# Performance work log

Measured on AMD Instinct MI355X. Metric: run time of the kernel, lower is better.

The kernel has to match this reference:

```python
import jax, jax.numpy as jnp
import numpy as np
from jax import lax

# config constants (match init_kwargs)
SEQ_LEN = 512
PRED_LEN = 96
ENC_IN = 64
D_MODEL = 128
E_LAYERS = 2
GRAPH_SCALE = 16
GRAPH_RANK = 8
TCN_KERNEL = 3
TCN_DILATION = 2
BATCH = 16


def setup_inputs() -> dict:
    key = jax.random.key(0)
    ks = jax.random.split(key, 12)
    s = 0.02
    inp = {
        "x_enc": jax.random.normal(ks[0], (BATCH, SEQ_LEN, ENC_IN), jnp.float32),
        "x_mark_enc": jnp.zeros((BATCH, SEQ_LEN, 4), jnp.float32),
        "x_dec": jnp.zeros((BATCH, PRED_LEN, ENC_IN), jnp.float32),
        "x_mark_dec": jnp.zeros((BATCH, PRED_LEN, 4), jnp.float32),
        # value embedding (scalar -> d_model)
        "w_emb": jax.random.normal(ks[1], (1, D_MODEL), jnp.float32) * s,
        "b_emb": jnp.zeros((D_MODEL,), jnp.float32),
        # stacked dilated causal conv layers [L, K, Cin, Cout]
        "conv_w": jax.random.normal(ks[2], (E_LAYERS, TCN_KERNEL, D_MODEL, D_MODEL), jnp.float32) * s,
        "conv_b": jnp.zeros((E_LAYERS, D_MODEL), jnp.float32),
        # low-rank graph generator projections
        "gg_w1": jax.random.normal(ks[3], (D_MODEL, GRAPH_RANK), jnp.float32) * s,
        "gg_b1": jnp.zeros((GRAPH_RANK,), jnp.float32),
        "gg_w2": jax.random.normal(ks[4], (D_MODEL, GRAPH_RANK), jnp.float32) * s,
        "gg_b2": jnp.zeros((GRAPH_RANK,), jnp.float32),
        # head: Linear(d_model * num_tokens, pred_len)
        "head_w": jax.random.normal(ks[5], (D_MODEL * SEQ_LEN, PRED_LEN), jnp.float32) * s,
        "head_b": jnp.zeros((PRED_LEN,), jnp.float32),
    }
    return inp


def _tcn(x_enc, w_emb, b_emb, conv_w, conv_b):
    # x_enc: [B, L, N] -> channel-independent per-variable encoding -> [B, N, L, D]
    B, L, N = x_enc.shape
    h = x_enc.transpose(0, 2, 1).reshape(B * N, L, 1) @ w_emb + b_emb  # [B*N, L, D]
    for i in range(conv_w.shape[0]):
        dil = TCN_DILATION ** i
        pad = (TCN_KERNEL - 1) * dil
        hp = jnp.pad(h, ((0, 0), (pad, 0), (0, 0)))  # causal left pad
        y = lax.conv_general_dilated(
            hp, conv_w[i], window_strides=(1,), padding="VALID",
            rhs_dilation=(dil,), dimension_numbers=("NWC", "WIO", "NWC"),
        ) + conv_b[i]
        h = jax.nn.gelu(y) + h  # residual
    return h.reshape(B, N, L, -1)


def _forward(x_enc, w_emb, b_emb, conv_w, conv_b, gg_w1, gg_b1, gg_w2, gg_b2, head_w, head_b):
    h_time = _tcn(x_enc, w_emb, b_emb, conv_w, conv_b)  # [B, N, L, D]
    B, N, L, D = h_time.shape
    S = L // GRAPH_SCALE  # number of segments (L divisible by scale)
    h_seg = h_time.reshape(B, N, S, GRAPH_SCALE, D)
    z = h_seg.mean(axis=3)  # [B, N, S, D] segment summaries
    # low-rank graph generation for all segments at once
    e1 = z @ gg_w1 + gg_b1  # [B, N, S, r]
    e2 = z @ gg_w2 + gg_b2
    scores = jnp.einsum("bnsr,bmsr->bsnm", e1, e2) / jnp.asarray(np.sqrt(GRAPH_RANK), z.dtype)
    adj = jax.nn.softmax(scores, axis=-1)  # [B, S, N, N] row-stochastic
    # adjacency temporal-smoothness regularizer: sum_s mean|adj_s - adj_{s-1}|
    reg = jnp.sum(jnp.mean(jnp.abs(adj[:, 1:] - adj[:, :-1]), axis=(0, 2, 3)))
    # graph-weighted feature mixing per segment
    h_mix = jnp.einsum("bsnm,bmscd->bnscd", adj, h_seg).reshape(B, N, L, D)
    # head over flattened (token, dim)
    out = h_mix.reshape(B, N, L * D) @ head_w + head_b  # [B, N, pred_len]
    return out.transpose(0, 2, 1), reg  # [B, pred_len, N]


def reference(x_enc, x_mark_enc, x_dec, x_mark_dec, w_emb, b_emb, conv_w, conv_b,
              gg_w1, gg_b1, gg_w2, gg_b2, head_w, head_b):
    # x_mark_enc / x_dec / x_mark_dec are unused by forecast path (faithful to source)
    return _forward(x_enc, w_emb, b_emb, conv_w, conv_b, gg_w1, gg_b1, gg_w2, gg_b2, head_w, head_b)
```

## Files before the change

kernel.cpp:

```cpp
#include <hip/hip_runtime.h>
#include <hip/hip_bf16.h>


#define BATCH 16
#define SEQ 512
#define NVAR 64
#define DM 128
#define SEG 32
#define SCL 16
#define RNK 8
#define PRED 96
#define BN (BATCH * NVAR)
#define ROWLEN (SEQ * DM)

typedef unsigned short ushort_t;
typedef __attribute__((ext_vector_type(8))) short short8;
typedef __attribute__((ext_vector_type(4))) float f32x4;

__device__ inline float bf2f(ushort_t u) {
    union { unsigned int i; float f; } x;
    x.i = ((unsigned int)u) << 16;
    return x.f;
}
__device__ inline ushort_t f2bf(float f) {
    union { float f; unsigned int i; } u;
    u.f = f;
    unsigned int x = u.i;
    return (ushort_t)((x + 0x7fffu + ((x >> 16) & 1u)) >> 16);
}
__device__ inline unsigned int pkbf(float a, float b) {
    __hip_bfloat162 h = __float22bfloat162_rn(make_float2(a, b));
    union { __hip_bfloat162 h2; unsigned int u; } c;
    c.h2 = h;
    return c.u;
}
__device__ inline float blo(unsigned int u) {
    union { unsigned int i; float f; } x;
    x.i = u << 16;
    return x.f;
}
__device__ inline float bhi(unsigned int u) {
    union { unsigned int i; float f; } x;
    x.i = u & 0xFFFF0000u;
    return x.f;
}
__device__ inline float gelu_fast(float x) {
    float t = 0.7978845608028654f * x * (1.0f + 0.044715f * x * x);
    float e = __expf(-2.0f * t);
    return x * __builtin_amdgcn_rcpf(1.0f + e);
}

__global__ __launch_bounds__(128) void wt_prep(
    const float* __restrict__ conv_w, ushort_t* __restrict__ WTf,
    float* __restrict__ regacc) {
    if (blockIdx.x == 0 && blockIdx.y == 0 && threadIdx.x == 0) regacc[0] = 0.f;
    int lt = blockIdx.x;
    int ci = blockIdx.y;
    int co = threadIdx.x;
    int kt = ci >> 5, quad = (ci >> 3) & 3, j = ci & 7;
    int ng = co >> 4, col = co & 15;
    int lane = quad * 16 + col;
    WTf[((((size_t)lt * 4 + kt) * 8 + ng) * 64 + lane) * 8 + j] =
        f2bf(conv_w[(size_t)lt * 16384 + (size_t)ci * 128 + co]);
}

__global__ __launch_bounds__(256, 4) void tcn_mfma(
    const float* __restrict__ x, const float* __restrict__ w_emb,
    const float* __restrict__ b_emb, const ushort_t* __restrict__ WTf,
    const float* __restrict__ conv_b,
    const float* __restrict__ gw1, const float* __restrict__ gb1,
    const float* __restrict__ gw2, const float* __restrict__ gb2,
    ushort_t* __restrict__ h2, float* __restrict__ e1, float* __restrict__ e2) {
    __shared__ __align__(16) ushort_t h0s[82 * 136];
    __shared__ __align__(16) ushort_t h1b[68 * 136];
    float* zb = reinterpret_cast<float*>(h1b);

    int bn = blockIdx.x;
    int b = bn >> 6, n = bn & 63;
    int chunk = blockIdx.y;
    int l0 = chunk * 64;

    {
        const float* xb = x + (size_t)b * SEQ * NVAR + n;
#pragma unroll
        for (int i = 0; i < 21; ++i) {
            int q = threadIdx.x + 256 * i;
            if (q < 82 * 64) {
                int row = q >> 6, dp = (q & 63) * 2;
                int l = l0 + row - 18;
                unsigned int pk = 0;
                if (l >= 0) {
                    float xv = xb[(size_t)l * NVAR];
                    float2 wv2 = *reinterpret_cast<const float2*>(&w_emb[dp]);
                    float2 bv2 = *reinterpret_cast<const float2*>(&b_emb[dp]);
                    pk = pkbf(xv * wv2.x + bv2.x, xv * wv2.y + bv2.y);
                }
                *reinterpret_cast<unsigned int*>(&h0s[row * 136 + dp]) = pk;
            }
        }
    }
    __syncthreads();

    int lane = threadIdx.x & 63;
    int wv = threadIdx.x >> 6;
    int quad = lane >> 4;
    int col = lane & 15;
    int cobase = wv * 32;

    f32x4 acc1[5][2];
#pragma unroll
    for (int mt = 0; mt < 5; ++mt)
#pragma unroll
        for (int nt = 0; nt < 2; ++nt)
            acc1[mt][nt] = (f32x4){0.f, 0.f, 0.f, 0.f};

#pragma unroll
    for (int tap = 0; tap < 3; ++tap) {
        short8 wf0[4], wf1[4];
#pragma unroll
        for (int kt = 0; kt < 4; ++kt) {
            const ushort_t* bp =
                WTf + ((((size_t)tap * 4 + kt) * 8 + wv * 2) * 64 + lane) * 8;
            wf0[kt] = *(const short8*)bp;
            wf1[kt] = *(const short8*)(bp + 512);
        }
#pragma unroll
        for (int kt = 0; kt < 4; ++kt) {
            int kc = kt * 32 + quad * 8;
#pragma unroll
            for (int mt = 0; mt < 5; ++mt) {
                short8 hf = *(const short8*)&h0s[(mt * 16 + col + tap) * 136 + kc];
                acc1[mt][0] = __builtin_amdgcn_mfma_f32_16x16x32_bf16(wf0[kt], hf, acc1[mt][0], 0, 0, 0);
                acc1[mt][1] = __builtin_amdgcn_mfma_f32_16x16x32_bf16(wf1[kt], hf, acc1[mt][1], 0, 0, 0);
            }
        }
    }
    {
        float4 bias[2];
        bias[0] = *reinterpret_cast<const float4*>(&conv_b[cobase + quad * 4]);
        bias[1] = *reinterpret_cast<const float4*>(&conv_b[cobase + 16 + quad * 4]);
#pragma unroll
        for (int mt = 0; mt < 5; ++mt) {
            int li = mt * 16 + col - 16;
            if (li >= -4) {
#pragma unroll
                for (int nt = 0; nt < 2; ++nt) {
                    int co = cobase + nt * 16 + quad * 4;
                    uint2 pk;
                    if (l0 + li < 0) {
                        pk.x = 0u; pk.y = 0u;
                    } else {
                        uint2 res = *reinterpret_cast<const uint2*>(
                            &h0s[(mt * 16 + col + 2) * 136 + co]);
                        float h0 = gelu_fast(acc1[mt][nt][0] + bias[nt].x) + blo(res.x);
                        float h1 = gelu_fast(acc1[mt][nt][1] + bias[nt].y) + bhi(res.x);
                        float h2v = gelu_fast(acc1[mt][nt][2] + bias[nt].z) + blo(res.y);
                        float h3 = gelu_fast(acc1[mt][nt][3] + bias[nt].w) + bhi(res.y);
                        pk.x = pkbf(h0, h1);
                        pk.y = pkbf(h2v, h3);
                    }
                    *reinterpret_cast<uint2*>(&h1b[(li + 4) * 136 + co]) = pk;
                }
            }
        }
    }
    __syncthreads();

    f32x4 acc2[4][2];
#pragma unroll
    for (int mt = 0; mt < 4; ++mt)
#pragma unroll
        for (int nt = 0; nt < 2; ++nt)
            acc2[mt][nt] = (f32x4){0.f, 0.f, 0.f, 0.f};

#pragma unroll
    for (int tap = 0; tap < 3; ++tap) {
        short8 wf0[4], wf1[4];
#pragma unroll
        for (int kt = 0; kt < 4; ++kt) {
            const ushort_t* bp =
                WTf + ((((size_t)(3 + tap) * 4 + kt) * 8 + wv * 2) * 64 + lane) * 8;
            wf0[kt] = *(const short8*)bp;
            wf1[kt] = *(const short8*)(bp + 512);
        }
#pragma unroll
        for (int kt = 0; kt < 4; ++kt) {
            int kc = kt * 32 + quad * 8;
#pragma unroll
            for (int mt = 0; mt < 4; ++mt) {
                short8 hf = *(const short8*)&h1b[(mt * 16 + col + 2 * tap) * 136 + kc];
                acc2[mt][0] = __builtin_amdgcn_mfma_f32_16x16x32_bf16(wf0[kt], hf, acc2[mt][0], 0, 0, 0);
                acc2[mt][1] = __builtin_amdgcn_mfma_f32_16x16x32_bf16(wf1[kt], hf, acc2[mt][1], 0, 0, 0);
            }
        }
    }
    {
        float4 bias[2];
        bias[0] = *reinterpret_cast<const float4*>(&conv_b[DM + cobase + quad * 4]);
        bias[1] = *reinterpret_cast<const float4*>(&conv_b[DM + cobase + 16 + quad * 4]);
#pragma unroll
        for (int mt = 0; mt < 4; ++mt) {
            int li = mt * 16 + col;
#pragma unroll
            for (int nt = 0; nt < 2; ++nt) {
                int co = cobase + nt * 16 + quad * 4;
                uint2 res = *reinterpret_cast<const uint2*>(
                    &h1b[(li + 4) * 136 + co]);
                float h0 = gelu_fast(acc2[mt][nt][0] + bias[nt].x) + blo(res.x);
                float h1 = gelu_fast(acc2[mt][nt][1] + bias[nt].y) + bhi(res.x);
                float h2v = gelu_fast(acc2[mt][nt][2] + bias[nt].z) + blo(res.y);
                float h3 = gelu_fast(acc2[mt][nt][3] + bias[nt].w) + bhi(res.y);
                uint2 pk;
                pk.x = pkbf(h0, h1);
                pk.y = pkbf(h2v, h3);
                *reinterpret_cast<uint2*>(&h0s[li * 136 + co]) = pk;
            }
        }
    }
    __syncthreads();

    {
        ushort_t* orow = h2 + (size_t)bn * ROWLEN + (size_t)l0 * 128;
#pragma unroll
        for (int i = 0; i < 4; ++i) {
            int q = threadIdx.x + 256 * i;
            int row = q >> 4, c8 = (q & 15) * 8;
            *(short8*)&orow[row * 128 + c8] = *(const short8*)&h0s[row * 136 + c8];
        }
    }
    {
        int d = threadIdx.x & 127, sg = threadIdx.x >> 7;
#pragma unroll
        for (int t = 0; t < 2; ++t) {
            int sl = sg + 2 * t;
            float a = 0.0f;
#pragma unroll
            for (int c = 0; c < SCL; ++c)
                a += bf2f(h0s[(sl * 16 + c) * 136 + d]);
            zb[sl * 128 + d] = a * (1.0f / 16.0f);
        }
    }
    __syncthreads();
    if (threadIdx.x < 64) {
        int sl = threadIdx.x >> 4;
        int which = (threadIdx.x >> 3) & 1;
        int r = threadIdx.x & 7;
        const float* w = which ? gw2 : gw1;
        float a = 0.0f;
        for (int d = 0; d < DM; ++d) a += zb[sl * 128 + d] * w[d * RNK + r];
        a += (which ? gb2 : gb1)[r];
        int s = chunk * 4 + sl;
        (which ? e2 : e1)[(((size_t)b * SEG + s) * NVAR + n) * RNK + r] = a;
    }
}

__global__ __launch_bounds__(256) void g_gemm(
    const ushort_t* __restrict__ h2, const float* __restrict__ head_w,
    float* __restrict__ G) {
    __shared__ __align__(16) ushort_t As[64 * 72];
    __shared__ __align__(16) ushort_t Bs[96 * 72];
    int s = blockIdx.x;
    int bnt = blockIdx.y;
    int kh = blockIdx.z;
    int bn0 = bnt * 64;
    int kbase = kh * 1024;
    int lane = threadIdx.x & 63, wv = threadIdx.x >> 6;
    int quad = lane >> 4, col = lane & 15;
    int mh = wv & 1;
    int ph = wv >> 1;

    int arow = threadIdx.x >> 2, akq = (threadIdx.x & 3) * 16;
    const ushort_t* aptr =
        h2 + (size_t)(bn0 + arow) * ROWLEN + (size_t)s * 2048 + kbase + akq;
    const float* bbase = head_w + ((size_t)s * 2048 + kbase) * PRED;
    int bp0[3], bk2[3];
#pragma unroll
    for (int i = 0; i < 3; ++i) {
        int q = threadIdx.x + 256 * i;
        bp0[i] = (q % 24) * 4;
        bk2[i] = (q / 24) * 2;
    }

    f32x4 acc[3][2];
#pragma unroll
    for (int i = 0; i < 3; ++i)
#pragma unroll
        for (int j = 0; j < 2; ++j) acc[i][j] = (f32x4){0.f, 0.f, 0.f, 0.f};

    short8 pa0 = *(const short8*)aptr;
    short8 pa1 = *(const short8*)(aptr + 8);
    float4 pb0[3], pb1[3];
#pragma unroll
    for (int i = 0; i < 3; ++i) {
        const float* src = bbase + (size_t)bk2[i] * PRED + bp0[i];
        pb0[i] = *reinterpret_cast<const float4*>(src);
        pb1[i] = *reinterpret_cast<const float4*>(src + PRED);
    }
    *(short8*)&As[arow * 72 + akq] = pa0;
    *(short8*)&As[arow * 72 + akq + 8] = pa1;
#pragma unroll
    for (int i = 0; i < 3; ++i) {
        *reinterpret_cast<unsigned int*>(&Bs[(bp0[i] + 0) * 72 + bk2[i]]) = pkbf(pb0[i].x, pb1[i].x);
        *reinterpret_cast<unsigned int*>(&Bs[(bp0[i] + 1) * 72 + bk2[i]]) = pkbf(pb0[i].y, pb1[i].y);
        *reinterpret_cast<unsigned int*>(&Bs[(bp0[i] + 2) * 72 + bk2[i]]) = pkbf(pb0[i].z, pb1[i].z);
        *reinterpret_cast<unsigned int*>(&Bs[(bp0[i] + 3) * 72 + bk2[i]]) = pkbf(pb0[i].w, pb1[i].w);
    }
    __syncthreads();

    for (int kt = 0; kt < 16; ++kt) {
        if (kt < 15) {
            const ushort_t* ap = aptr + (kt + 1) * 64;
            pa0 = *(const short8*)ap;
            pa1 = *(const short8*)(ap + 8);
#pragma unroll
            for (int i = 0; i < 3; ++i) {
                const float* src =
                    bbase + (size_t)((kt + 1) * 64 + bk2[i]) * PRED + bp0[i];
                pb0[i] = *reinterpret_cast<const float4*>(src);
                pb1[i] = *reinterpret_cast<const float4*>(src + PRED);
            }
        }
#pragma unroll
        for (int kk = 0; kk < 2; ++kk) {
            int kc = kk * 32 + quad * 8;
            short8 pfr[3];
#pragma unroll
            for (int i = 0; i < 3; ++i)
                pfr[i] = *(const short8*)&Bs[(ph * 48 + i * 16 + col) * 72 + kc];
#pragma unroll
            for (int j = 0; j < 2; ++j) {
                short8 bnfr = *(const short8*)&As[(mh * 32 + j * 16 + col) * 72 + kc];
#pragma unroll
                for (int i = 0; i < 3; ++i)
                    acc[i][j] = __builtin_amdgcn_mfma_f32_16x16x32_bf16(pfr[i], bnfr, acc[i][j], 0, 0, 0);
            }
        }
        __syncthreads();
        if (kt < 15) {
            *(short8*)&As[arow * 72 + akq] = pa0;
            *(short8*)&As[arow * 72 + akq + 8] = pa1;
#pragma unroll
            for (int i = 0; i < 3; ++i) {
                *reinterpret_cast<unsigned int*>(&Bs[(bp0[i] + 0) * 72 + bk2[i]]) = pkbf(pb0[i].x, pb1[i].x);
                *reinterpret_cast<unsigned int*>(&Bs[(bp0[i] + 1) * 72 + bk2[i]]) = pkbf(pb0[i].y, pb1[i].y);
                *reinterpret_cast<unsigned int*>(&Bs[(bp0[i] + 2) * 72 + bk2[i]]) = pkbf(pb0[i].z, pb1[i].z);
                *reinterpret_cast<unsigned int*>(&Bs[(bp0[i] + 3) * 72 + bk2[i]]) = pkbf(pb0[i].w, pb1[i].w);
            }
            __syncthreads();
        }
    }
    int b = bnt;
#pragma unroll
    for (int i = 0; i < 3; ++i)
#pragma unroll
        for (int j = 0; j < 2; ++j)
#pragma unroll
            for (int r = 0; r < 4; ++r) {
                int p = ph * 48 + i * 16 + quad * 4 + r;
                int m = mh * 32 + j * 16 + col;
                atomicAdd(&G[(((size_t)s * BATCH + b) * PRED + p) * NVAR + m],
                          acc[i][j][r]);
            }
}

__global__ __launch_bounds__(256) void out_partial(
    const float* __restrict__ e1, const float* __restrict__ e2,
    const float* __restrict__ G, float* __restrict__ partial,
    float* __restrict__ regacc) {
    __shared__ float adjn[2][32][65];
    __shared__ float Gs[96][65];
    __shared__ float e2s[3][64][8];
    __shared__ float e1s[3][32][8];
    __shared__ float wsum[4];
    int b = blockIdx.x, sg = blockIdx.y, nh = blockIdx.z;
    int s0 = sg * 2;
    int wv = threadIdx.x >> 6, lane = threadIdx.x & 63;

    for (int idx = threadIdx.x; idx < 3 * 64 * 8; idx += 256) {
        int j = idx >> 9, m = (idx >> 3) & 63, r = idx & 7;
        int s = s0 - 1 + j;
        e2s[j][m][r] = (s >= 0)
            ? e2[(((size_t)b * SEG + s) * NVAR + m) * RNK + r] : 0.0f;
    }
    for (int idx = threadIdx.x; idx < 3 * 32 * 8; idx += 256) {
        int j = idx >> 8, nl = (idx >> 3) & 31, r = idx & 7;
        int s = s0 - 1 + j;
        e1s[j][nl][r] = (s >= 0)
            ? e1[(((size_t)b * SEG + s) * NVAR + nh * 32 + nl) * RNK + r] : 0.0f;
    }
    __syncthreads();

    float regsum = 0.0f;
    for (int t = 0; t < 8; ++t) {
        int nl = wv * 8 + t;
        float a[3];
#pragma unroll
        for (int j = 0; j < 3; ++j) {
            float sc = 0.0f;
#pragma unroll
            for (int r = 0; r < 8; ++r) sc += e1s[j][nl][r] * e2s[j][lane][r];
            sc *= 0.35355339059327373f;
            float mx = sc;
            for (int off = 32; off; off >>= 1)
                mx = fmaxf(mx, __shfl_xor(mx, off, 64));
            float ex = __expf(sc - mx);
            float sm = ex;
            for (int off = 32; off; off >>= 1) sm += __shfl_xor(sm, off, 64);
            a[j] = ex * __builtin_amdgcn_rcpf(sm);
        }
        if (s0 > 0) regsum += fabsf(a[1] - a[0]);
        regsum += fabsf(a[2] - a[1]);
        adjn[0][nl][lane] = a[1];
        adjn[1][nl][lane] = a[2];
    }
    __syncthreads();

    int pg = threadIdx.x >> 4;
    int ng = threadIdx.x & 15;
    float acc[6][2];
#pragma unroll
    for (int j = 0; j < 6; ++j) { acc[j][0] = 0.f; acc[j][1] = 0.f; }

#pragma unroll
    for (int ss = 0; ss < 2; ++ss) {
        int s = s0 + ss;
#pragma unroll
        for (int i = 0; i < 6; ++i) {
            int q = threadIdx.x + 256 * i;
            int row = q >> 4, mq = (q & 15) * 4;
            float4 v = *reinterpret_cast<const float4*>(
                &G[(((size_t)s * BATCH + b) * PRED + row) * NVAR + mq]);
            Gs[row][mq + 0] = v.x; Gs[row][mq + 1] = v.y;
            Gs[row][mq + 2] = v.z; Gs[row][mq + 3] = v.w;
        }
        __syncthreads();
#pragma unroll 4
        for (int m = 0; m < 64; ++m) {
            float a0 = adjn[ss][ng * 2 + 0][m];
            float a1 = adjn[ss][ng * 2 + 1][m];
#pragma unroll
            for (int j = 0; j < 6; ++j) {
                float g = Gs[pg * 6 + j][m];
                acc[j][0] += g * a0;
                acc[j][1] += g * a1;
            }
        }
        __syncthreads();
    }
#pragma unroll
    for (int j = 0; j < 6; ++j)
#pragma unroll
        for (int i = 0; i < 2; ++i) {
            int p = pg * 6 + j, n = nh * 32 + ng * 2 + i;
            partial[(((size_t)sg * BATCH + b) * PRED + p) * NVAR + n] = acc[j][i];
        }
    for (int off = 32; off; off >>= 1) regsum += __shfl_xor(regsum, off, 64);
    if (lane == 0) wsum[wv] = regsum;
    __syncthreads();
    if (threadIdx.x == 0)
        atomicAdd(regacc, wsum[0] + wsum[1] + wsum[2] + wsum[3]);
}

__global__ __launch_bounds__(256) void out_reduce(
    const float* __restrict__ partial, const float* __restrict__ head_b,
    const float* __restrict__ regacc, float* __restrict__ out, int out_size) {
    int i4 = blockIdx.x * 256 + threadIdx.x;
    int p = (i4 >> 4) % PRED;
    float hb = head_b[p];
    float4 a = make_float4(hb, hb, hb, hb);
    const int stride4 = BATCH * PRED * NVAR / 4;
    const float4* p4 = reinterpret_cast<const float4*>(partial);
#pragma unroll
    for (int sg = 0; sg < 16; ++sg) {
        float4 v = p4[sg * stride4 + i4];
        a.x += v.x; a.y += v.y; a.z += v.z; a.w += v.w;
    }
    reinterpret_cast<float4*>(out)[i4] = a;
    if (i4 == 0) out[out_size - 1] = regacc[0] * (1.0f / 65536.0f);
}

extern "C" void kernel_launch(void* const* d_in, const int* in_sizes, int n_in,
                              void* d_out, int out_size, void* d_ws,
                              size_t ws_size, hipStream_t stream) {
    const float* x_enc  = (const float*)d_in[0];
    const float* w_emb  = (const float*)d_in[4];
    const float* b_emb  = (const float*)d_in[5];
    const float* conv_w = (const float*)d_in[6];
    const float* conv_b = (const float*)d_in[7];
    const float* gg_w1  = (const float*)d_in[8];
    const float* gg_b1  = (const float*)d_in[9];
    const float* gg_w2  = (const float*)d_in[10];
    const float* gg_b2  = (const float*)d_in[11];
    const float* head_w = (const float*)d_in[12];
    const float* head_b = (const float*)d_in[13];
    float* out = (float*)d_out;

    char* ws = (char*)d_ws;
    ushort_t* h2   = (ushort_t*)(ws);
    float* partial = (float*)(ws);
    float* G       = (float*)(ws + 134217728);
    float* e1      = (float*)(ws + 146800640);
    float* e2      = (float*)(ws + 147849216);
    ushort_t* WTf  = (ushort_t*)(ws + 148897792);
    float* regacc  = (float*)(ws + 157286400);

    hipMemsetAsync(G, 0, 12582912, stream);
    wt_prep<<<dim3(6, 128), 128, 0, stream>>>(conv_w, WTf, regacc);
    tcn_mfma<<<dim3(BN, SEQ / 64), 256, 0, stream>>>(
        x_enc, w_emb, b_emb, WTf, conv_b,
        gg_w1, gg_b1, gg_w2, gg_b2, h2, e1, e2);
    g_gemm<<<dim3(SEG, BATCH, 2), 256, 0, stream>>>(h2, head_w, G);
    out_partial<<<dim3(BATCH, 16, 2), 256, 0, stream>>>(
        e1, e2, G, partial, regacc);
    out_reduce<<<BATCH * PRED * NVAR / 1024, 256, 0, stream>>>(
        partial, head_b, regacc, out, out_size);
}
```

Baseline: 364.1 us.

## Retile TCN conv MFMA work across waves by channel half and row group

```diff
diff --git a/kernel.cpp b/kernel.cpp
--- a/kernel.cpp
+++ b/kernel.cpp
@@ -105,104 +105,117 @@
     int wv = threadIdx.x >> 6;
     int quad = lane >> 4;
     int col = lane & 15;
-    int cobase = wv * 32;
-
-    f32x4 acc1[5][2];
-#pragma unroll
-    for (int mt = 0; mt < 5; ++mt)
-#pragma unroll
-        for (int nt = 0; nt < 2; ++nt)
+    int ch = wv & 1;
+    int lg = wv >> 1;
+    int cobase = ch * 64;
+
+    f32x4 acc1[3][4];
+#pragma unroll
+    for (int mt = 0; mt < 3; ++mt)
+#pragma unroll
+        for (int nt = 0; nt < 4; ++nt)
             acc1[mt][nt] = (f32x4){0.f, 0.f, 0.f, 0.f};
+    int mtc1 = lg ? 2 : 3;
+    int rb1 = lg * 48;
 
 #pragma unroll
     for (int tap = 0; tap < 3; ++tap) {
-        short8 wf0[4], wf1[4];
 #pragma unroll
         for (int kt = 0; kt < 4; ++kt) {
-            const ushort_t* bp =
-                WTf + ((((size_t)tap * 4 + kt) * 8 + wv * 2) * 64 + lane) * 8;
-            wf0[kt] = *(const short8*)bp;
-            wf1[kt] = *(const short8*)(bp + 512);
-        }
+            short8 wf[4];
+#pragma unroll
+            for (int nt = 0; nt < 4; ++nt)
+                wf[nt] = *(const short8*)(WTf +
+                    ((((size_t)tap * 4 + kt) * 8 + ch * 4 + nt) * 64 + lane) * 8);
+            int kc = kt * 32 + quad * 8;
+#pragma unroll
+            for (int mt = 0; mt < 3; ++mt) {
+                if (mt < mtc1) {
+                    short8 hf = *(const short8*)&h0s[
+                        (rb1 + mt * 16 + col + tap) * 136 + kc];
+#pragma unroll
+                    for (int nt = 0; nt < 4; ++nt)
+                        acc1[mt][nt] = __builtin_amdgcn_mfma_f32_16x16x32_bf16(
+                            wf[nt], hf, acc1[mt][nt], 0, 0, 0);
+                }
+            }
+        }
+    }
+    {
+        float4 bias[4];
+#pragma unroll
+        for (int nt = 0; nt < 4; ++nt)
+            bias[nt] = *reinterpret_cast<const float4*>(
+                &conv_b[cobase + nt * 16 + quad * 4]);
+#pragma unroll
+        for (int mt = 0; mt < 3; ++mt) {
+            if (mt < mtc1) {
+                int li = rb1 + mt * 16 + col - 16;
+                if (li >= -4) {
+#pragma unroll
+                    for (int nt = 0; nt < 4; ++nt) {
+                        int co = cobase + nt * 16 + quad * 4;
+                        uint2 pk;
+                        if (l0 + li < 0) {
+                            pk.x = 0u; pk.y = 0u;
+                        } else {
+                            uint2 res = *reinterpret_cast<const uint2*>(
+                                &h0s[(li + 18) * 136 + co]);
+                            float h0 = gelu_fast(acc1[mt][nt][0] + bias[nt].x) + blo(res.x);
+                            float h1 = gelu_fast(acc1[mt][nt][1] + bias[nt].y) + bhi(res.x);
+                            float h2v = gelu_fast(acc1[mt][nt][2] + bias[nt].z) + blo(res.y);
+                            float h3 = gelu_fast(acc1[mt][nt][3] + bias[nt].w) + bhi(res.y);
+                            pk.x = pkbf(h0, h1);
+                            pk.y = pkbf(h2v, h3);
+                        }
+                        *reinterpret_cast<uint2*>(&h1b[(li + 4) * 136 + co]) = pk;
+                    }
+                }
+            }
+        }
+    }
+    __syncthreads();
+
+    f32x4 acc2[2][4];
+#pragma unroll
+    for (int mt = 0; mt < 2; ++mt)
+#pragma unroll
+        for (int nt = 0; nt < 4; ++nt)
+            acc2[mt][nt] = (f32x4){0.f, 0.f, 0.f, 0.f};
+    int rb2 = lg * 32;
+
+#pragma unroll
+    for (int tap = 0; tap < 3; ++tap) {
 #pragma unroll
         for (int kt = 0; kt < 4; ++kt) {
+            short8 wf[4];
+#pragma unroll
+            for (int nt = 0; nt < 4; ++nt)
+                wf[nt] = *(const short8*)(WTf +
+                    ((((size_t)(3 + tap) * 4 + kt) * 8 + ch * 4 + nt) * 64 + lane) * 8);
             int kc = kt * 32 + quad * 8;
 #pragma unroll
-            for (int mt = 0; mt < 5; ++mt) {
-                short8 hf = *(const short8*)&h0s[(mt * 16 + col + tap) * 136 + kc];
-                acc1[mt][0] = __builtin_amdgcn_mfma_f32_16x16x32_bf16(wf0[kt], hf, acc1[mt][0], 0, 0, 0);
-                acc1[mt][1] = __builtin_amdgcn_mfma_f32_16x16x32_bf16(wf1[kt], hf, acc1[mt][1], 0, 0, 0);
+            for (int mt = 0; mt < 2; ++mt) {
+                short8 hf = *(const short8*)&h1b[
+                    (rb2 + mt * 16 + col + 2 * tap) * 136 + kc];
+#pragma unroll
+                for (int nt = 0; nt < 4; ++nt)
+                    acc2[mt][nt] = __builtin_amdgcn_mfma_f32_16x16x32_bf16(
+                        wf[nt], hf, acc2[mt][nt], 0, 0, 0);
             }
         }
     }
     {
-        float4 bias[2];
-        bias[0] = *reinterpret_cast<const float4*>(&conv_b[cobase + quad * 4]);
-        bias[1] = *reinterpret_cast<const float4*>(&conv_b[cobase + 16 + quad * 4]);
-#pragma unroll
-        for (int mt = 0; mt < 5; ++mt) {
-            int li = mt * 16 + col - 16;
-            if (li >= -4) {
-#pragma unroll
-                for (int nt = 0; nt < 2; ++nt) {
-                    int co = cobase + nt * 16 + quad * 4;
-                    uint2 pk;
-                    if (l0 + li < 0) {
-                        pk.x = 0u; pk.y = 0u;
-                    } else {
-                        uint2 res = *reinterpret_cast<const uint2*>(
-                            &h0s[(mt * 16 + col + 2) * 136 + co]);
-                        float h0 = gelu_fast(acc1[mt][nt][0] + bias[nt].x) + blo(res.x);
-                        float h1 = gelu_fast(acc1[mt][nt][1] + bias[nt].y) + bhi(res.x);
-                        float h2v = gelu_fast(acc1[mt][nt][2] + bias[nt].z) + blo(res.y);
-                        float h3 = gelu_fast(acc1[mt][nt][3] + bias[nt].w) + bhi(res.y);
-                        pk.x = pkbf(h0, h1);
-                        pk.y = pkbf(h2v, h3);
-                    }
-                    *reinterpret_cast<uint2*>(&h1b[(li + 4) * 136 + co]) = pk;
-                }
-            }
-        }
-    }
-    __syncthreads();
-
-    f32x4 acc2[4][2];
-#pragma unroll
-    for (int mt = 0; mt < 4; ++mt)
-#pragma unroll
-        for (int nt = 0; nt < 2; ++nt)
-            acc2[mt][nt] = (f32x4){0.f, 0.f, 0.f, 0.f};
-
-#pragma unroll
-    for (int tap = 0; tap < 3; ++tap) {
-        short8 wf0[4], wf1[4];
-#pragma unroll
-        for (int kt = 0; kt < 4; ++kt) {
-            const ushort_t* bp =
-                WTf + ((((size_t)(3 + tap) * 4 + kt) * 8 + wv * 2) * 64 + lane) * 8;
-            wf0[kt] = *(const short8*)bp;
-            wf1[kt] = *(const short8*)(bp + 512);
-        }
-#pragma unroll
-        for (int kt = 0; kt < 4; ++kt) {
-            int kc = kt * 32 + quad * 8;
-#pragma unroll
-            for (int mt = 0; mt < 4; ++mt) {
-                short8 hf = *(const short8*)&h1b[(mt * 16 + col + 2 * tap) * 136 + kc];
-                acc2[mt][0] = __builtin_amdgcn_mfma_f32_16x16x32_bf16(wf0[kt], hf, acc2[mt][0], 0, 0, 0);
-                acc2[mt][1] = __builtin_amdgcn_mfma_f32_16x16x32_bf16(wf1[kt], hf, acc2[mt][1], 0, 0, 0);
-            }
-        }
-    }
-    {
-        float4 bias[2];
-        bias[0] = *reinterpret_cast<const float4*>(&conv_b[DM + cobase + quad * 4]);
-        bias[1] = *reinterpret_cast<const float4*>(&conv_b[DM + cobase + 16 + quad * 4]);
-#pragma unroll
-        for (int mt = 0; mt < 4; ++mt) {
-            int li = mt * 16 + col;
-#pragma unroll
-            for (int nt = 0; nt < 2; ++nt) {
+        float4 bias[4];
+#pragma unroll
+        for (int nt = 0; nt < 4; ++nt)
+            bias[nt] = *reinterpret_cast<const float4*>(
+                &conv_b[DM + cobase + nt * 16 + quad * 4]);
+#pragma unroll
+        for (int mt = 0; mt < 2; ++mt) {
+            int li = rb2 + mt * 16 + col;
+#pragma unroll
+            for (int nt = 0; nt < 4; ++nt) {
                 int co = cobase + nt * 16 + quad * 4;
                 uint2 res = *reinterpret_cast<const uint2*>(
                     &h1b[(li + 4) * 136 + co]);
@@ -229,16 +242,18 @@
         }
     }
     {
-        int d = threadIdx.x & 127, sg = threadIdx.x >> 7;
-#pragma unroll
-        for (int t = 0; t < 2; ++t) {
-            int sl = sg + 2 * t;
-            float a = 0.0f;
-#pragma unroll
-            for (int c = 0; c < SCL; ++c)
-                a += bf2f(h0s[(sl * 16 + c) * 136 + d]);
-            zb[sl * 128 + d] = a * (1.0f / 16.0f);
-        }
+        int d2 = (threadIdx.x & 63) * 2;
+        int sg = threadIdx.x >> 6;
+        float a0 = 0.0f, a1 = 0.0f;
+#pragma unroll
+        for (int c = 0; c < SCL; ++c) {
+            unsigned int v = *reinterpret_cast<const unsigned int*>(
+                &h0s[(sg * 16 + c) * 136 + d2]);
+            a0 += blo(v);
+            a1 += bhi(v);
+        }
+        zb[sg * 128 + d2] = a0 * (1.0f / 16.0f);
+        zb[sg * 128 + d2 + 1] = a1 * (1.0f / 16.0f);
     }
     __syncthreads();
     if (threadIdx.x < 64) {
```

After: 402.6 us. 10.6% more time.
